# Kernel optimization log

Measured on AMD Instinct MI355X. Metric: run time of the kernel, lower is better.

## Reference

```python
import jax, jax.numpy as jnp
import numpy as np

# pywt Wavelet('db4') filter bank (8 taps)
_DEC_LO = np.array([-0.010597401785069032, 0.032883011666982945, 0.030841381835986965,
                    -0.18703481171888114, -0.02798376941698385, 0.6308807679295904,
                    0.7148465705525415, 0.23037781330885523], dtype=np.float32)
_REC_LO = _DEC_LO[::-1].copy()
_DEC_HI = (np.array([(-1.0) ** (k + 1) for k in range(8)], dtype=np.float32) * _REC_LO)
_REC_HI = _DEC_HI[::-1].copy()
_FLEN = 8
_LEVEL = 3


def _corr(x, filt, stride):
    # x: (N, L); cross-correlation with `filt`, VALID, given stride -> (N, Lout)
    k = jnp.asarray(filt.copy())[None, None, :].astype(x.dtype)
    y = jax.lax.conv_general_dilated(x[:, None, :], k, (stride,), 'VALID',
                                     dimension_numbers=('NCH', 'OIH', 'NCH'))
    return y[:, 0, :]


def _dwt(x):
    # pywt dwt, mode='symmetric': pad F-1 each side, full convolution, keep odd phase
    p = _FLEN - 1
    ext = jnp.pad(x, ((0, 0), (p, p)), mode='symmetric')[:, 1:]
    cA = _corr(ext, _DEC_LO[::-1], 2)  # conv == corr with flipped filter
    cD = _corr(ext, _DEC_HI[::-1], 2)
    return cA, cD


def _idwt(a, d):
    # pywt idwt: upsample by 2 (values at even idx), full conv, trim F-2 each side
    n = a.shape[-1]

    def up(c):
        # upsampled (2n-1) with 1 zero of padding on each side -> length 2n+1
        u = jnp.zeros((c.shape[0], 2 * n + 1), c.dtype)
        return u.at[:, 1::2].set(c)

    return _corr(up(a), _REC_LO[::-1], 1) + _corr(up(d), _REC_HI[::-1], 1)


def _waverec(a, details):
    # details ordered coarsest -> finest (as pywt waverec consumes them)
    for d in details:
        if a.shape[-1] == d.shape[-1] + 1:
            a = a[:, :-1]
        a = _idwt(a, d)
    return a


def setup_inputs() -> dict:
    key = jax.random.key(0)
    x = jax.random.normal(key, (32, 64, 16384), dtype=jnp.float32)
    return {"x": x}


def reference(x):
    B, F, L = x.shape
    x2 = x.reshape(B * F, L)

    # wavedec: repeatedly split the approximation
    a = x2
    details = []  # finest first
    for _ in range(_LEVEL):
        a, d = _dwt(a)
        details.append(d)
    details = details[::-1]  # coarsest -> finest, matching waverec order

    low = _waverec(a, [jnp.zeros_like(d) for d in details])
    high = _waverec(jnp.zeros_like(a), details)

    low = low[:, :L].reshape(B, F, L)
    high = high[:, :L].reshape(B, F, L)
    return (low, high)
```

## Files before the change

kernel.cpp:

```cpp
#include <hip/hip_runtime.h>

namespace {
constexpr int kL0 = 16384;
constexpr int kN1 = 8195;
constexpr int kN2 = 4101;
constexpr int kThreads = 128;
constexpr int kTS = 1024;
constexpr int kTilesPerRow = kL0 / kTS;

constexpr int SXF = 1120;
constexpr int SA1 = 554;
constexpr int SA2 = 274;
constexpr int SA3 = 134;

constexpr float RLc[8] = {
     0.23037781330885523f,  0.7148465705525415f,   0.6308807679295904f,
    -0.02798376941698385f, -0.18703481171888114f,  0.030841381835986965f,
     0.032883011666982945f, -0.010597401785069032f };

struct WT { float w[8][7]; };
constexpr WT make_w() {
    WT W{};
    for (int r = 0; r < 8; ++r) {
        const int r2 = r >> 1, pi = r & 1;
        for (int u = 0; u < 4; ++u) {
            const float cu = RLc[6 + pi - 2 * u];
            const int k = r2 + u, k2 = k >> 1, pk = k & 1;
            for (int s = 0; s < 4; ++s) {
                const float cs = RLc[6 + pk - 2 * s];
                const int j = k2 + s, j2 = j >> 1, pj = j & 1;
                for (int t = 0; t < 4; ++t)
                    W.w[r][j2 + t] += cu * cs * RLc[6 + pj - 2 * t];
            }
        }
    }
    return W;
}

__device__ constexpr float RL[8] = {
     0.23037781330885523f,  0.7148465705525415f,   0.6308807679295904f,
    -0.02798376941698385f, -0.18703481171888114f,  0.030841381835986965f,
     0.032883011666982945f, -0.010597401785069032f };
__device__ constexpr WT W = make_w();
}

__device__ __forceinline__ int reflect(int g, int N) {
    if (g < 0)  g = -1 - g;
    if (g >= N) g = 2 * N - 1 - g;
    return g;
}

__device__ __forceinline__ float tap8f2(const float* __restrict__ p) {
    const float2* q = reinterpret_cast<const float2*>(p);
    const float2 q0 = q[0], q1 = q[1], q2 = q[2], q3 = q[3];
    float s = q0.x * RL[0];
    s = fmaf(q0.y, RL[1], s); s = fmaf(q1.x, RL[2], s); s = fmaf(q1.y, RL[3], s);
    s = fmaf(q2.x, RL[4], s); s = fmaf(q2.y, RL[5], s); s = fmaf(q3.x, RL[6], s);
    s = fmaf(q3.y, RL[7], s);
    return s;
}

__device__ __forceinline__ void bar_lgkm() {
    asm volatile("s_waitcnt lgkmcnt(0)" ::: "memory");
    __builtin_amdgcn_s_barrier();
    asm volatile("" ::: "memory");
}
__device__ __forceinline__ void bar_full() {
    asm volatile("s_waitcnt vmcnt(0) lgkmcnt(0)" ::: "memory");
    __builtin_amdgcn_s_barrier();
    asm volatile("" ::: "memory");
}

__global__ void __launch_bounds__(kThreads, 8)
wavelet_v14(const float* __restrict__ x, float* __restrict__ out, int rows) {
    __shared__ __align__(16) float sx [SXF];
    __shared__ __align__(16) float sa1[SA1 + 2];
    __shared__ __align__(16) float sa2[SA2 + 2];
    __shared__ __align__(16) float sa3[SA3 + 2];

    const int tid  = threadIdx.x;
    const int row  = blockIdx.x >> 4;
    const int tile = blockIdx.x & 15;
    const int O    = tile << 10;
    const int XB   = O - 44;
    const int A0   = (O >> 1) - 18;
    const int B0   = (O >> 2) - 6;
    const float* __restrict__ xr = x + (size_t)row * kL0;
    const bool edge = (tile == 0) || (tile == kTilesPerRow - 1);

    const float4* xr4 = reinterpret_cast<const float4*>(xr + O + 8 * tid);
    const float4 xv0 = xr4[0], xv1 = xr4[1];

    if (!edge) {
        #pragma unroll
        for (int pass = 0; pass < 2; ++pass) {
            const int m0 = 4 * tid + (pass << 9);
            if (m0 < SA1) {
                const float4* __restrict__ p =
                    reinterpret_cast<const float4*>(xr + (O - 44 + 2 * m0));
                const float4 u = p[0], v = p[1], w2 = p[2], z = p[3];
                const float e[16] = {u.x, u.y, u.z, u.w, v.x, v.y, v.z, v.w,
                                     w2.x, w2.y, w2.z, w2.w, z.x, z.y, z.z, z.w};
                float o[4];
                #pragma unroll
                for (int i = 0; i < 4; ++i) {
                    float s = e[2 + 2 * i] * RL[0];
                    #pragma unroll
                    for (int k = 1; k < 8; ++k)
                        s = fmaf(e[2 + 2 * i + k], RL[k], s);
                    o[i] = s;
                }
                if (m0 + 3 < SA1) {
                    *reinterpret_cast<float4*>(&sa1[m0]) =
                        make_float4(o[0], o[1], o[2], o[3]);
                } else {
                    #pragma unroll
                    for (int i = 0; i < 4; ++i)
                        if (m0 + i < SA1) sa1[m0 + i] = o[i];
                }
            }
        }
        bar_lgkm();

        sa2[tid]       = tap8f2(&sa1[2 * tid]);
        sa2[tid + 128] = tap8f2(&sa1[2 * (tid + 128)]);
        if (tid < SA2 - 256) {
            const int m = 256 + tid;
            sa2[m] = tap8f2(&sa1[2 * m]);
        }
        bar_lgkm();

        sa3[tid] = tap8f2(&sa2[2 * tid]);
        if (tid < SA3 - 128) {
            const int m = 128 + tid;
            sa3[m] = tap8f2(&sa2[2 * m]);
        }
        bar_lgkm();
    } else {
        const int t0  = (tile == 0) ? 44 : 4;
        const int thi = (tile == 0) ? 1116 : 1068;
        const int Nv  = (thi - t0) >> 2;
        for (int v = tid; v < Nv; v += kThreads) {
            const float4 val = *reinterpret_cast<const float4*>(xr + XB + t0 + 4 * v);
            sx[t0 + 4 * v]     = val.x; sx[t0 + 4 * v + 1] = val.y;
            sx[t0 + 4 * v + 2] = val.z; sx[t0 + 4 * v + 3] = val.w;
        }
        for (int t = 2 + tid; t < 1116; t += kThreads)
            if (t < t0 || t >= thi)
                sx[t] = xr[reflect(XB + t, kL0)];
        bar_full();

        for (int m = tid; m < SA1; m += kThreads) {
            const int g  = A0 + m;
            const int mh = (g >= 0 && g < kN1) ? m : (reflect(g, kN1) - A0);
            sa1[m] = tap8f2(&sx[2 * mh + 2]);
        }
        bar_lgkm();

        for (int m = tid; m < SA2; m += kThreads) {
            const int g = B0 + m;
            const int j = (g >= 0 && g < kN2) ? m : (reflect(g, kN2) - B0);
            sa2[m] = tap8f2(&sa1[2 * j]);
        }
        bar_lgkm();

        for (int m = tid; m < SA3; m += kThreads)
            sa3[m] = tap8f2(&sa2[2 * m]);
        bar_lgkm();
    }

    {
        float a[7];
        #pragma unroll
        for (int m = 0; m < 7; ++m) a[m] = sa3[tid + m];
        float lo[8];
        #pragma unroll
        for (int r = 0; r < 8; ++r) {
            float s = a[0] * W.w[r][0];
            #pragma unroll
            for (int m = 1; m < 7; ++m) s = fmaf(a[m], W.w[r][m], s);
            lo[r] = s;
        }
        float* __restrict__ lowp  = out + (size_t)row * kL0 + O + 8 * tid;
        float* __restrict__ highp = lowp + (size_t)rows * kL0;
        reinterpret_cast<float4*>(lowp)[0]  = make_float4(lo[0], lo[1], lo[2], lo[3]);
        reinterpret_cast<float4*>(lowp)[1]  = make_float4(lo[4], lo[5], lo[6], lo[7]);
        reinterpret_cast<float4*>(highp)[0] = make_float4(xv0.x - lo[0], xv0.y - lo[1],
                                                          xv0.z - lo[2], xv0.w - lo[3]);
        reinterpret_cast<float4*>(highp)[1] = make_float4(xv1.x - lo[4], xv1.y - lo[5],
                                                          xv1.z - lo[6], xv1.w - lo[7]);
    }
}

extern "C" void kernel_launch(void* const* d_in, const int* in_sizes, int n_in,
                              void* d_out, int out_size, void* d_ws, size_t ws_size,
                              hipStream_t stream) {
    (void)n_in; (void)d_ws; (void)ws_size; (void)out_size;
    const float* x = (const float*)d_in[0];
    float* out = (float*)d_out;
    const int rows = in_sizes[0] / kL0;
    const int blocks = rows * kTilesPerRow;
    hipLaunchKernelGGL(wavelet_v14, dim3(blocks), dim3(kThreads), 0, stream,
                       x, out, rows);
}
```

Baseline: 89.89 us.

## Fuse first two analysis levels in registers and use nontemporal output stores

In interior tiles, each thread now loads 28 consecutive input floats, computes ten level-1 approximation values in registers, and derives two level-2 values directly. This removes the sa1 shared-memory round trip and one barrier. The cost is redundant level-1 work (overlapping windows across threads) and wider per-thread global loads. Output stores are switched to nontemporal vector stores to reduce cache pollution on the large streaming write.

```diff
diff --git a/kernel.cpp b/kernel.cpp
--- a/kernel.cpp
+++ b/kernel.cpp
@@ -42,6 +42,8 @@
     -0.02798376941698385f, -0.18703481171888114f,  0.030841381835986965f,
      0.032883011666982945f, -0.010597401785069032f };
 __device__ constexpr WT W = make_w();
+
+typedef float vfloat4 __attribute__((ext_vector_type(4)));
 }
 
 __device__ __forceinline__ int reflect(int g, int N) {
@@ -72,7 +74,7 @@
 }
 
 __global__ void __launch_bounds__(kThreads, 8)
-wavelet_v14(const float* __restrict__ x, float* __restrict__ out, int rows) {
+wavelet_v15(const float* __restrict__ x, float* __restrict__ out, int rows) {
     __shared__ __align__(16) float sx [SXF];
     __shared__ __align__(16) float sa1[SA1 + 2];
     __shared__ __align__(16) float sa2[SA2 + 2];
@@ -94,39 +96,37 @@
     if (!edge) {
         #pragma unroll
         for (int pass = 0; pass < 2; ++pass) {
-            const int m0 = 4 * tid + (pass << 9);
-            if (m0 < SA1) {
+            const int m0 = (pass == 0) ? (2 * tid) : (256 + 2 * tid);
+            if (pass == 0 || tid < 9) {
                 const float4* __restrict__ p =
-                    reinterpret_cast<const float4*>(xr + (O - 44 + 2 * m0));
-                const float4 u = p[0], v = p[1], w2 = p[2], z = p[3];
-                const float e[16] = {u.x, u.y, u.z, u.w, v.x, v.y, v.z, v.w,
-                                     w2.x, w2.y, w2.z, w2.w, z.x, z.y, z.z, z.w};
-                float o[4];
+                    reinterpret_cast<const float4*>(xr + XB + 4 * m0);
+                float e[28];
                 #pragma unroll
-                for (int i = 0; i < 4; ++i) {
-                    float s = e[2 + 2 * i] * RL[0];
+                for (int c = 0; c < 7; ++c) {
+                    const float4 v = p[c];
+                    e[4 * c] = v.x; e[4 * c + 1] = v.y;
+                    e[4 * c + 2] = v.z; e[4 * c + 3] = v.w;
+                }
+                float a1r[10];
+                #pragma unroll
+                for (int u = 0; u < 10; ++u) {
+                    float s = e[2 * u + 2] * RL[0];
                     #pragma unroll
                     for (int k = 1; k < 8; ++k)
-                        s = fmaf(e[2 + 2 * i + k], RL[k], s);
+                        s = fmaf(e[2 * u + 2 + k], RL[k], s);
+                    a1r[u] = s;
+                }
+                float o[2];
+                #pragma unroll
+                for (int i = 0; i < 2; ++i) {
+                    float s = a1r[2 * i] * RL[0];
+                    #pragma unroll
+                    for (int k = 1; k < 8; ++k)
+                        s = fmaf(a1r[2 * i + k], RL[k], s);
                     o[i] = s;
                 }
-                if (m0 + 3 < SA1) {
-                    *reinterpret_cast<float4*>(&sa1[m0]) =
-                        make_float4(o[0], o[1], o[2], o[3]);
-                } else {
-                    #pragma unroll
-                    for (int i = 0; i < 4; ++i)
-                        if (m0 + i < SA1) sa1[m0 + i] = o[i];
-                }
+                *reinterpret_cast<float2*>(&sa2[m0]) = make_float2(o[0], o[1]);
             }
-        }
-        bar_lgkm();
-
-        sa2[tid]       = tap8f2(&sa1[2 * tid]);
-        sa2[tid + 128] = tap8f2(&sa1[2 * (tid + 128)]);
-        if (tid < SA2 - 256) {
-            const int m = 256 + tid;
-            sa2[m] = tap8f2(&sa1[2 * m]);
         }
         bar_lgkm();
 
@@ -183,12 +183,14 @@
         }
         float* __restrict__ lowp  = out + (size_t)row * kL0 + O + 8 * tid;
         float* __restrict__ highp = lowp + (size_t)rows * kL0;
-        reinterpret_cast<float4*>(lowp)[0]  = make_float4(lo[0], lo[1], lo[2], lo[3]);
-        reinterpret_cast<float4*>(lowp)[1]  = make_float4(lo[4], lo[5], lo[6], lo[7]);
-        reinterpret_cast<float4*>(highp)[0] = make_float4(xv0.x - lo[0], xv0.y - lo[1],
-                                                          xv0.z - lo[2], xv0.w - lo[3]);
-        reinterpret_cast<float4*>(highp)[1] = make_float4(xv1.x - lo[4], xv1.y - lo[5],
-                                                          xv1.z - lo[6], xv1.w - lo[7]);
+        vfloat4 l0 = {lo[0], lo[1], lo[2], lo[3]};
+        vfloat4 l1 = {lo[4], lo[5], lo[6], lo[7]};
+        vfloat4 h0 = {xv0.x - lo[0], xv0.y - lo[1], xv0.z - lo[2], xv0.w - lo[3]};
+        vfloat4 h1 = {xv1.x - lo[4], xv1.y - lo[5], xv1.z - lo[6], xv1.w - lo[7]};
+        __builtin_nontemporal_store(l0, reinterpret_cast<vfloat4*>(lowp));
+        __builtin_nontemporal_store(l1, reinterpret_cast<vfloat4*>(lowp) + 1);
+        __builtin_nontemporal_store(h0, reinterpret_cast<vfloat4*>(highp));
+        __builtin_nontemporal_store(h1, reinterpret_cast<vfloat4*>(highp) + 1);
     }
 }
 
@@ -200,6 +202,6 @@
     float* out = (float*)d_out;
     const int rows = in_sizes[0] / kL0;
     const int blocks = rows * kTilesPerRow;
-    hipLaunchKernelGGL(wavelet_v14, dim3(blocks), dim3(kThreads), 0, stream,
+    hipLaunchKernelGGL(wavelet_v15, dim3(blocks), dim3(kThreads), 0, stream,
                        x, out, rows);
 }
```

Result: faster. 82.30 us (-8.4%).
